# Kernel tuning notes

Hardware: AMD Instinct MI355X
Metric: run time of the kernel (lower is better)

The kernel has to match this reference:

```python
import jax, jax.numpy as jnp
import numpy as np
import math

EMB = 2048
HEADS = 16
HEAD_DIM = EMB // HEADS  # 128
SCALE = math.sqrt(HEAD_DIM)


def srms_norm(x, eps_min=1e-12):
    # Scaled RMS norm over last dim, computed in float32.
    d = x.shape[-1]
    xf = x.astype(jnp.float32)
    norm = jnp.linalg.norm(xf * (1.0 / math.sqrt(d)), axis=-1, keepdims=True)
    norm = jnp.maximum(norm, eps_min)
    return (xf / norm).astype(x.dtype)


def setup_inputs() -> dict:
    key = jax.random.key(0)
    ks = jax.random.split(key, 6)
    x = jax.random.normal(ks[0], (4, 4096, EMB), dtype=jnp.float32)
    # xavier-normal std for square D x D: sqrt(2/(D+D)) = 1/sqrt(D); gain=1 (lth=None)
    std = 1.0 / math.sqrt(EMB)
    Wq = jax.random.normal(ks[1], (EMB, EMB), dtype=jnp.float32) * std
    Wk = jax.random.normal(ks[2], (EMB, EMB), dtype=jnp.float32) * std
    Wv = jax.random.normal(ks[3], (EMB, EMB), dtype=jnp.float32) * std
    Wu = jax.random.normal(ks[4], (EMB, EMB), dtype=jnp.float32) * std
    Wo = jax.random.normal(ks[5], (EMB, EMB), dtype=jnp.float32) * std
    return {"x": x, "Wq": Wq, "Wk": Wk, "Wv": Wv, "Wu": Wu, "Wo": Wo}


def reference(x, Wq, Wk, Wv, Wu, Wo):
    B, L, D = x.shape
    H, dh = HEADS, HEAD_DIM
    # projections (weights stored as [in, out])
    q = (x @ Wq).reshape(B, L, H, dh).transpose(0, 2, 1, 3)  # [B,H,L,dh]
    k = (x @ Wk).reshape(B, L, H, dh).transpose(0, 2, 1, 3)
    v = (x @ Wv).reshape(B, L, H, dh).transpose(0, 2, 1, 3)
    u = (x @ Wu).reshape(B, L, H, dh).transpose(0, 2, 1, 3)
    q = jax.nn.relu(q) / SCALE
    k = jax.nn.relu(k) / SCALE
    u = jax.nn.silu(u)
    # linear retention: kv state [B,H,dh,dh], then q @ kv
    kv = jnp.einsum('bhlk,bhlv->bhkv', k, v)
    out = jnp.einsum('bhlk,bhkv->bhlv', q, kv)
    out = srms_norm(out) * u
    out = out.transpose(0, 2, 1, 3).reshape(B, L, D)
    return out @ Wo
```

## Files before the change

kernel.cpp:

```cpp
#include <hip/hip_runtime.h>
#include <hip/hip_bf16.h>
#include <cstdint>


typedef __attribute__((ext_vector_type(8))) short short8;
typedef __attribute__((ext_vector_type(4))) float f32x4;

#define DEVI static __device__ __forceinline__

DEVI float bf2f(unsigned short u) {
    union { unsigned int i; float f; } w; w.i = ((unsigned int)u) << 16; return w.f;
}
DEVI unsigned short f2bf(float f) {
    union { float f; unsigned int i; } w; w.f = f;
    return (unsigned short)((w.i + 0x7fffu + ((w.i >> 16) & 1u)) >> 16);
}

#define GLDS16(gp, lp) __builtin_amdgcn_global_load_lds( \
    (const __attribute__((address_space(1))) void*)(gp), \
    (__attribute__((address_space(3))) void*)(lp), 16, 0, 0)

__global__ void probe_dtype(const unsigned short* __restrict__ x, int* flag) {
    __shared__ int cnt;
    if (threadIdx.x == 0) cnt = 0;
    __syncthreads();
    int c = 0;
    for (int i = threadIdx.x; i < 4096; i += 256) {
        float a = fabsf(bf2f(x[i]));
        if (!(a <= 1e4f) || (a != 0.0f && a < 1e-4f)) ++c;
    }
    atomicAdd(&cnt, c);
    __syncthreads();
    if (threadIdx.x == 0) *flag = (cnt < 512) ? 1 : 0;
}

__global__ void wconvert(const void* __restrict__ Wq, const void* __restrict__ Wk,
                         const void* __restrict__ Wv, const void* __restrict__ Wu,
                         const void* __restrict__ Wo,
                         unsigned short* __restrict__ wt4,
                         unsigned short* __restrict__ wot,
                         const int* __restrict__ flag) {
    const int z = blockIdx.z;
    const void* W = (z == 0) ? Wq : (z == 1) ? Wk : (z == 2) ? Wv : (z == 3) ? Wu : Wo;
    const bool isbf = (*flag != 0);
    __shared__ float tile[32][33];
    const int j0 = blockIdx.x * 32, i0 = blockIdx.y * 32;
    const int tx = threadIdx.x, ty = threadIdx.y;
#pragma unroll
    for (int r = 0; r < 4; ++r) {
        const int i = i0 + ty * 4 + r;
        float v;
        if (isbf) v = bf2f(((const unsigned short*)W)[i * 2048 + j0 + tx]);
        else      v = ((const float*)W)[i * 2048 + j0 + tx];
        tile[ty * 4 + r][tx] = v;
    }
    __syncthreads();
#pragma unroll
    for (int r = 0; r < 4; ++r) {
        const int j = j0 + ty * 4 + r;
        const unsigned short bv = f2bf(tile[tx][ty * 4 + r]);
        if (z < 4) wt4[(long)(z * 2048 + j) * 2048 + i0 + tx] = bv;
        else       wot[(long)j * 2048 + i0 + tx] = bv;
    }
}

__global__ void xconvert(const void* __restrict__ X, unsigned short* __restrict__ xb,
                         const int* __restrict__ flag) {
    const bool isbf = (*flag != 0);
    const long i = (long)blockIdx.x * 256 + threadIdx.x;
    if (isbf) {
        ((uint4*)xb)[i] = ((const uint4*)X)[i];
    } else {
        const float4 f0 = ((const float4*)X)[2 * i];
        const float4 f1 = ((const float4*)X)[2 * i + 1];
        union { unsigned short us[8]; uint4 v; } o;
        o.us[0] = f2bf(f0.x); o.us[1] = f2bf(f0.y); o.us[2] = f2bf(f0.z); o.us[3] = f2bf(f0.w);
        o.us[4] = f2bf(f1.x); o.us[5] = f2bf(f1.y); o.us[6] = f2bf(f1.z); o.us[7] = f2bf(f1.w);
        ((uint4*)xb)[i] = o.v;
    }
}

DEVI void gemm_core(const unsigned short* __restrict__ Ag,
                    const unsigned short* __restrict__ Bg,
                    unsigned short* As, unsigned short* Bs,
                    f32x4 acc[8][4], const int tid) {
    const int wave = tid >> 6, lane = tid & 63;
    const int wr = wave >> 2, wc = wave & 3;
    const int srow = tid >> 2;
    const int lsl = (tid & 3) ^ ((srow >> 1) & 3);
    const unsigned short* ga0 = Ag + (long)srow * 2048 + lsl * 8;
    const unsigned short* ga1 = ga0 + 128 * 2048;
    const unsigned short* gb0 = Bg + (long)srow * 2048 + lsl * 8;
    const unsigned short* gb1 = gb0 + 128 * 2048;
    const int ldsb = wave * 512;

    const int psl = ((lane >> 4) ^ (((lane & 15) >> 1) & 3)) * 8;
    const int abase = (wr * 128 + (lane & 15)) * 32 + psl;
    const int bbase = (wc * 64 + (lane & 15)) * 32 + psl;

#define ISSUE(tt) do { const int _b = (tt) & 3; const int _ko = (tt) * 32; \
    GLDS16(ga0 + _ko, As + _b * 8192 + ldsb); \
    GLDS16(ga1 + _ko, As + _b * 8192 + 4096 + ldsb); \
    GLDS16(gb0 + _ko, Bs + _b * 8192 + ldsb); \
    GLDS16(gb1 + _ko, Bs + _b * 8192 + 4096 + ldsb); } while (0)
#define RDFRAG(aX, bX, buf) do { \
    const unsigned short* _a = As + (buf) * 8192; \
    const unsigned short* _b = Bs + (buf) * 8192; \
    _Pragma("unroll") for (int fm = 0; fm < 8; ++fm) aX[fm] = *(const short8*)(_a + abase + fm * 512); \
    _Pragma("unroll") for (int fn = 0; fn < 4; ++fn) bX[fn] = *(const short8*)(_b + bbase + fn * 512); } while (0)
#define MFMACL(aX, bX) do { \
    __builtin_amdgcn_s_setprio(1); \
    _Pragma("unroll") for (int fm = 0; fm < 8; ++fm) \
    _Pragma("unroll") for (int fn = 0; fn < 4; ++fn) \
        acc[fm][fn] = __builtin_amdgcn_mfma_f32_16x16x32_bf16(aX[fm], bX[fn], acc[fm][fn], 0, 0, 0); \
    __builtin_amdgcn_s_setprio(0); } while (0)

    ISSUE(0); ISSUE(1); ISSUE(2); ISSUE(3);
    asm volatile("s_waitcnt vmcnt(12)" ::: "memory");
    asm volatile("s_barrier" ::: "memory");
    short8 aE[8], bE[4], aO[8], bO[4];
    RDFRAG(aE, bE, 0);

    for (int tp = 0; tp < 32; ++tp) {
        const int t = 2 * tp;
        asm volatile("s_waitcnt vmcnt(8)" ::: "memory");
        asm volatile("s_barrier" ::: "memory");
        RDFRAG(aO, bO, (t + 1) & 3);
        asm volatile("s_waitcnt lgkmcnt(12)" ::: "memory");
        { int ti = t + 4; if (ti >= 64) ti -= 64; ISSUE(ti); }
        MFMACL(aE, bE);
        asm volatile("s_waitcnt vmcnt(8)" ::: "memory");
        asm volatile("s_barrier" ::: "memory");
        { int tr = t + 2; if (tr > 63) tr = 63; RDFRAG(aE, bE, tr & 3); }
        asm volatile("s_waitcnt lgkmcnt(12)" ::: "memory");
        { int ti = t + 5; if (ti >= 64) ti -= 64; ISSUE(ti); }
        MFMACL(aO, bO);
    }
    asm volatile("s_waitcnt vmcnt(0) lgkmcnt(0)" ::: "memory");
#undef ISSUE
#undef RDFRAG
#undef MFMACL
}

__global__ __launch_bounds__(512, 2)
void gemm_qkvu(const unsigned short* __restrict__ Xb,
               const unsigned short* __restrict__ Wt4,
               unsigned short* __restrict__ Qb, unsigned short* __restrict__ Kb,
               unsigned short* __restrict__ Vb, unsigned short* __restrict__ Ub) {
    __shared__ unsigned short As[4 * 8192];
    __shared__ unsigned short Bs[4 * 8192];
    const int orig = blockIdx.x;
    const int flat = (orig & 7) * 256 + (orig >> 3);
    const int mt = flat & 63, nt = flat >> 6;
    const long m0 = (long)mt * 256;
    const int tid = threadIdx.x;
    f32x4 acc[8][4] = {};

    gemm_core(Xb + m0 * 2048, Wt4 + (long)nt * 256 * 2048, As, Bs, acc, tid);

    const int wave = tid >> 6, lane = tid & 63;
    const int wr = wave >> 2, wc = wave & 3;
    const int seg = nt >> 3;
    unsigned short* outp = (seg == 0) ? Qb : (seg == 1) ? Kb : (seg == 2) ? Vb : Ub;
    const int cl0 = (nt & 7) * 256 + wc * 64;
#pragma unroll
    for (int fm = 0; fm < 8; ++fm) {
#pragma unroll
        for (int fn = 0; fn < 4; ++fn) {
            const int col = cl0 + fn * 16 + (lane & 15);
#pragma unroll
            for (int r = 0; r < 4; ++r) {
                const long row = m0 + wr * 128 + fm * 16 + ((lane >> 4) << 2) + r;
                float v = acc[fm][fn][r];
                if (seg <= 1)      v = fmaxf(v, 0.0f) * 0.08838834764831845f;
                else if (seg == 3) v = v / (1.0f + __expf(-v));
                outp[row * 2048 + col] = f2bf(v);
            }
        }
    }
}

__global__ __launch_bounds__(512, 2)
void gemm_out(const unsigned short* __restrict__ Obuf,
              const unsigned short* __restrict__ Wot,
              void* __restrict__ out, const int* __restrict__ flag) {
    __shared__ unsigned short As[4 * 8192];
    __shared__ unsigned short Bs[4 * 8192];
    const int orig = blockIdx.x;
    const int flat = (orig & 7) * 64 + (orig >> 3);
    const int mt = flat & 63, nt = flat >> 6;
    const long m0 = (long)mt * 256;
    const int j0 = nt * 256;
    const int tid = threadIdx.x;
    f32x4 acc[8][4] = {};

    gemm_core(Obuf + m0 * 2048, Wot + (long)j0 * 2048, As, Bs, acc, tid);

    const int wave = tid >> 6, lane = tid & 63;
    const int wr = wave >> 2, wc = wave & 3;
    const bool isbf = (*flag != 0);
#pragma unroll
    for (int fm = 0; fm < 8; ++fm) {
#pragma unroll
        for (int fn = 0; fn < 4; ++fn) {
            const int col = j0 + wc * 64 + fn * 16 + (lane & 15);
#pragma unroll
            for (int r = 0; r < 4; ++r) {
                const long row = m0 + wr * 128 + fm * 16 + ((lane >> 4) << 2) + r;
                const float v = acc[fm][fn][r];
                if (isbf) ((unsigned short*)out)[row * 2048 + col] = f2bf(v);
                else      ((float*)out)[row * 2048 + col] = v;
            }
        }
    }
}

__global__ void kv_accum(const unsigned short* __restrict__ Kb,
                         const unsigned short* __restrict__ Vb,
                         float* __restrict__ KVpart) {
    __shared__ unsigned short Kt[128 * 64];
    __shared__ unsigned short Vt[128 * 64];
    const int bh = blockIdx.x;
    const int chunk = blockIdx.y;
    const int b = bh >> 4, h = bh & 15;
    const int t = threadIdx.x, wave = t >> 6, lane = t & 63;
    const int wr = wave >> 1, wc = wave & 1;
    const int l0 = (t & 15) * 4;
    const int dkg = t >> 4;
    const long gbase = ((long)b * 4096 + chunk * 1024) * 2048 + h * 128;
    f32x4 acc[4][4] = {};

    for (int tile = 0; tile < 16; ++tile) {
        __syncthreads();
        short8 kr[4], vr[4];
#pragma unroll
        for (int li = 0; li < 4; ++li) {
            const long go = gbase + (long)(tile * 64 + l0 + li) * 2048 + dkg * 8;
            kr[li] = *(const short8*)(Kb + go);
            vr[li] = *(const short8*)(Vb + go);
        }
#pragma unroll
        for (int i = 0; i < 8; ++i) {
            const int row = dkg * 8 + i;
            const int lin = row * 128 + l0 * 2;
            const int off = (lin ^ ((row & 7) << 4)) >> 1;
            union { unsigned short us[4]; unsigned long long u; } pk, pv;
#pragma unroll
            for (int li = 0; li < 4; ++li) { pk.us[li] = (unsigned short)kr[li][i]; pv.us[li] = (unsigned short)vr[li][i]; }
            *(unsigned long long*)(Kt + off) = pk.u;
            *(unsigned long long*)(Vt + off) = pv.u;
        }
        __syncthreads();
#pragma unroll
        for (int ks = 0; ks < 2; ++ks) {
            const int kof = ks * 64 + (lane >> 4) * 16;
            short8 a[4], bfr[4];
#pragma unroll
            for (int f = 0; f < 4; ++f) {
                const int ra = wr * 64 + f * 16 + (lane & 15);
                const int rb = wc * 64 + f * 16 + (lane & 15);
                a[f]   = *(const short8*)(Vt + (((ra * 128 + kof) ^ ((ra & 7) << 4)) >> 1));
                bfr[f] = *(const short8*)(Kt + (((rb * 128 + kof) ^ ((rb & 7) << 4)) >> 1));
            }
#pragma unroll
            for (int fm = 0; fm < 4; ++fm)
#pragma unroll
                for (int fn = 0; fn < 4; ++fn)
                    acc[fm][fn] = __builtin_amdgcn_mfma_f32_16x16x32_bf16(a[fm], bfr[fn], acc[fm][fn], 0, 0, 0);
        }
    }
    float* dst = KVpart + ((long)chunk * 64 + bh) * 16384;
#pragma unroll
    for (int fm = 0; fm < 4; ++fm)
#pragma unroll
        for (int fn = 0; fn < 4; ++fn)
#pragma unroll
            for (int r = 0; r < 4; ++r) {
                const int dv = wr * 64 + fm * 16 + ((lane >> 4) << 2) + r;
                const int dk = wc * 64 + fn * 16 + (lane & 15);
                dst[dv * 128 + dk] = acc[fm][fn][r];
            }
}

__global__ void kv_finalize(const float* __restrict__ KVpart,
                            unsigned short* __restrict__ KVhi) {
    const long base = ((long)blockIdx.x * 256 + threadIdx.x) * 4;
    float4 s0 = *(const float4*)(KVpart + base);
    const float4 s1 = *(const float4*)(KVpart + 1048576 + base);
    const float4 s2 = *(const float4*)(KVpart + 2097152 + base);
    const float4 s3 = *(const float4*)(KVpart + 3145728 + base);
    float s[4] = { s0.x + s1.x + s2.x + s3.x, s0.y + s1.y + s2.y + s3.y,
                   s0.z + s1.z + s2.z + s3.z, s0.w + s1.w + s2.w + s3.w };
    union { unsigned short us[4]; unsigned long long u; } hi;
#pragma unroll
    for (int j = 0; j < 4; ++j) hi.us[j] = f2bf(s[j]);
    *(unsigned long long*)(KVhi + base) = hi.u;
}

__global__ void o_norm(const unsigned short* __restrict__ Qb,
                       const unsigned short* __restrict__ Ub,
                       const unsigned short* __restrict__ KVhi,
                       unsigned short* __restrict__ Ob) {
    __shared__ unsigned short Qs[128 * 128];
    const int tid = threadIdx.x, wave = tid >> 6, lane = tid & 63;
    const int tile = blockIdx.x;
    const int bh = blockIdx.y;
    const int b = bh >> 4, h = bh & 15;
    const long n0 = (long)b * 4096 + tile * 128;

    const int qrow = tid >> 4;
    const int qcol = (tid & 15) * 8;
#pragma unroll
    for (int i = 0; i < 8; ++i)
        GLDS16(Qb + (n0 + i * 16 + qrow) * 2048 + h * 128 + qcol, Qs + i * 2048 + wave * 512);
    __syncthreads();

    const unsigned short* KH = KVhi + (long)bh * 16384;
    f32x4 acc[2][8] = {};
#pragma unroll
    for (int kk = 0; kk < 4; ++kk) {
        const short8 a0 = *(const short8*)(Qs + (wave * 32 + (lane & 15)) * 128 + kk * 32 + (lane >> 4) * 8);
        const short8 a1 = *(const short8*)(Qs + (wave * 32 + 16 + (lane & 15)) * 128 + kk * 32 + (lane >> 4) * 8);
#pragma unroll
        for (int fn = 0; fn < 8; ++fn) {
            const int bo = (fn * 16 + (lane & 15)) * 128 + kk * 32 + (lane >> 4) * 8;
            const short8 bhi = *(const short8*)(KH + bo);
            acc[0][fn] = __builtin_amdgcn_mfma_f32_16x16x32_bf16(a0, bhi, acc[0][fn], 0, 0, 0);
            acc[1][fn] = __builtin_amdgcn_mfma_f32_16x16x32_bf16(a1, bhi, acc[1][fn], 0, 0, 0);
        }
    }

#pragma unroll
    for (int fm = 0; fm < 2; ++fm) {
#pragma unroll
        for (int r = 0; r < 4; ++r) {
            float ssq = 0.0f;
#pragma unroll
            for (int fn = 0; fn < 8; ++fn) { const float v = acc[fm][fn][r]; ssq += v * v; }
            ssq += __shfl_xor(ssq, 1);
            ssq += __shfl_xor(ssq, 2);
            ssq += __shfl_xor(ssq, 4);
            ssq += __shfl_xor(ssq, 8);
            const float nrm = fmaxf(sqrtf(ssq) * 0.08838834764831845f, 1e-12f);
            const float scl = 1.0f / nrm;
            const long row = n0 + wave * 32 + fm * 16 + ((lane >> 4) << 2) + r;
#pragma unroll
            for (int fn = 0; fn < 8; ++fn) {
                const int col = fn * 16 + (lane & 15);
                const float uv = bf2f(Ub[row * 2048 + h * 128 + col]);
                Ob[row * 2048 + h * 128 + col] = f2bf(acc[fm][fn][r] * scl * uv);
            }
        }
    }
}

extern "C" void kernel_launch(void* const* d_in, const int* in_sizes, int n_in,
                              void* d_out, int out_size, void* d_ws, size_t ws_size,
                              hipStream_t stream) {
    (void)in_sizes; (void)n_in; (void)out_size; (void)ws_size;
    char* ws = (char*)d_ws;
    unsigned short* Xb  = (unsigned short*)(ws + 0);
    unsigned short* Wt4 = (unsigned short*)(ws + 67108864);
    unsigned short* Wot = (unsigned short*)(ws + 100663296);
    unsigned short* Qb  = (unsigned short*)(ws + 109051904);
    unsigned short* Kb  = (unsigned short*)(ws + 176160768);
    unsigned short* Vb  = (unsigned short*)(ws + 243269632);
    unsigned short* Ub  = (unsigned short*)(ws + 310378496);
    int*            flag= (int*)(ws + 381681664);
    float*          KVpart = (float*)Wt4;
    unsigned short* KVhi   = (unsigned short*)(ws + 67108864 + 16777216);
    unsigned short* Ob     = Xb;

    probe_dtype<<<1, 256, 0, stream>>>((const unsigned short*)d_in[0], flag);
    wconvert<<<dim3(64, 64, 5), dim3(32, 8), 0, stream>>>(d_in[1], d_in[2], d_in[3],
                                                          d_in[4], d_in[5], Wt4, Wot, flag);
    xconvert<<<16384, 256, 0, stream>>>(d_in[0], Xb, flag);
    gemm_qkvu<<<2048, 512, 0, stream>>>(Xb, Wt4, Qb, Kb, Vb, Ub);
    kv_accum<<<dim3(64, 4), 256, 0, stream>>>(Kb, Vb, KVpart);
    kv_finalize<<<1024, 256, 0, stream>>>(KVpart, KVhi);
    o_norm<<<dim3(32, 64), 256, 0, stream>>>(Qb, Ub, KVhi, Ob);
    gemm_out<<<512, 512, 0, stream>>>(Ob, Wot, d_out, flag);
}
```

Before: 979.4 us.

## Stage GEMM and norm epilogues through swizzled LDS for vectorized stores

The QKVU and output GEMM epilogues now write accumulator fragments into XOR-swizzled shared memory (reusing the A/B tiles) and then emit 16-byte coalesced global stores instead of scattered 2- or 4-byte stores. The o_norm kernel loads U into LDS with global_load_lds, swizzles the Q/U tiles, and writes its output through LDS with vector stores. kv_accum changes its thread mapping and swizzle to cut LDS bank conflicts. This adds barriers and extra LDS traffic in exchange for far fewer, wider global memory transactions.

```diff
diff --git a/kernel.cpp b/kernel.cpp
--- a/kernel.cpp
+++ b/kernel.cpp
@@ -163,20 +163,33 @@
     const int seg = nt >> 3;
     unsigned short* outp = (seg == 0) ? Qb : (seg == 1) ? Kb : (seg == 2) ? Vb : Ub;
     const int cl0 = (nt & 7) * 256 + wc * 64;
+
+    __syncthreads();
+    unsigned short* reg = (wave < 4 ? As : Bs) + (wave & 3) * 8192;
 #pragma unroll
     for (int fm = 0; fm < 8; ++fm) {
 #pragma unroll
         for (int fn = 0; fn < 4; ++fn) {
-            const int col = cl0 + fn * 16 + (lane & 15);
 #pragma unroll
             for (int r = 0; r < 4; ++r) {
-                const long row = m0 + wr * 128 + fm * 16 + ((lane >> 4) << 2) + r;
+                const int lrow = fm * 16 + ((lane >> 4) << 2) + r;
+                const int lcol = fn * 16 + (lane & 15);
                 float v = acc[fm][fn][r];
                 if (seg <= 1)      v = fmaxf(v, 0.0f) * 0.08838834764831845f;
                 else if (seg == 3) v = v / (1.0f + __expf(-v));
-                outp[row * 2048 + col] = f2bf(v);
+                const int ofs = lrow * 64 + ((((lcol >> 3) ^ ((lrow >> 2) & 7)) << 3) | (lcol & 7));
+                reg[ofs] = f2bf(v);
             }
         }
+    }
+#pragma unroll
+    for (int p = 0; p < 16; ++p) {
+        const int row = p * 8 + (lane >> 3);
+        const int slotL = lane & 7;
+        const uint4 val = *(const uint4*)(reg + row * 64 + slotL * 8);
+        const long grow = m0 + wr * 128 + row;
+        const int gcol = cl0 + ((slotL ^ ((row >> 2) & 7)) << 3);
+        *(uint4*)(outp + grow * 2048 + gcol) = val;
     }
 }
 
@@ -199,17 +212,57 @@
     const int wave = tid >> 6, lane = tid & 63;
     const int wr = wave >> 2, wc = wave & 3;
     const bool isbf = (*flag != 0);
-#pragma unroll
-    for (int fm = 0; fm < 8; ++fm) {
-#pragma unroll
-        for (int fn = 0; fn < 4; ++fn) {
-            const int col = j0 + wc * 64 + fn * 16 + (lane & 15);
-#pragma unroll
-            for (int r = 0; r < 4; ++r) {
-                const long row = m0 + wr * 128 + fm * 16 + ((lane >> 4) << 2) + r;
-                const float v = acc[fm][fn][r];
-                if (isbf) ((unsigned short*)out)[row * 2048 + col] = f2bf(v);
-                else      ((float*)out)[row * 2048 + col] = v;
+    __syncthreads();
+    unsigned short* reg = (wave < 4 ? As : Bs) + (wave & 3) * 8192;
+
+    if (isbf) {
+        unsigned short* outp = (unsigned short*)out;
+        const int cl0 = j0 + wc * 64;
+#pragma unroll
+        for (int fm = 0; fm < 8; ++fm)
+#pragma unroll
+            for (int fn = 0; fn < 4; ++fn)
+#pragma unroll
+                for (int r = 0; r < 4; ++r) {
+                    const int lrow = fm * 16 + ((lane >> 4) << 2) + r;
+                    const int lcol = fn * 16 + (lane & 15);
+                    const int ofs = lrow * 64 + ((((lcol >> 3) ^ ((lrow >> 2) & 7)) << 3) | (lcol & 7));
+                    reg[ofs] = f2bf(acc[fm][fn][r]);
+                }
+#pragma unroll
+        for (int p = 0; p < 16; ++p) {
+            const int row = p * 8 + (lane >> 3);
+            const int slotL = lane & 7;
+            const uint4 val = *(const uint4*)(reg + row * 64 + slotL * 8);
+            const long grow = m0 + wr * 128 + row;
+            const int gcol = cl0 + ((slotL ^ ((row >> 2) & 7)) << 3);
+            *(uint4*)(outp + grow * 2048 + gcol) = val;
+        }
+    } else {
+        float* outf = (float*)out;
+        float* regf = (float*)reg;
+#pragma unroll
+        for (int h = 0; h < 2; ++h) {
+#pragma unroll
+            for (int fm = 0; fm < 8; ++fm)
+#pragma unroll
+                for (int fnh = 0; fnh < 2; ++fnh)
+#pragma unroll
+                    for (int r = 0; r < 4; ++r) {
+                        const int fn = h * 2 + fnh;
+                        const int lrow = fm * 16 + ((lane >> 4) << 2) + r;
+                        const int lcolf = fnh * 16 + (lane & 15);
+                        const int ofs = lrow * 32 + ((((lcolf >> 2) ^ ((lrow >> 2) & 7)) << 2) | (lcolf & 3));
+                        regf[ofs] = acc[fm][fn][r];
+                    }
+#pragma unroll
+            for (int p = 0; p < 16; ++p) {
+                const int row = p * 8 + (lane >> 3);
+                const int slotL = lane & 7;
+                const float4 val = *(const float4*)(regf + row * 32 + slotL * 4);
+                const long grow = m0 + wr * 128 + row;
+                const int gcol = j0 + wc * 64 + h * 32 + ((slotL ^ ((row >> 2) & 7)) << 2);
+                *(float4*)(outf + grow * 2048 + gcol) = val;
             }
         }
     }
@@ -225,8 +278,8 @@
     const int b = bh >> 4, h = bh & 15;
     const int t = threadIdx.x, wave = t >> 6, lane = t & 63;
     const int wr = wave >> 1, wc = wave & 1;
-    const int l0 = (t & 15) * 4;
-    const int dkg = t >> 4;
+    const int dkg = t & 15;
+    const int l0 = (t >> 4) * 4;
     const long gbase = ((long)b * 4096 + chunk * 1024) * 2048 + h * 128;
     f32x4 acc[4][4] = {};
 
@@ -243,7 +296,7 @@
         for (int i = 0; i < 8; ++i) {
             const int row = dkg * 8 + i;
             const int lin = row * 128 + l0 * 2;
-            const int off = (lin ^ ((row & 7) << 4)) >> 1;
+            const int off = (lin ^ ((((row) ^ (row >> 3)) & 7) << 4)) >> 1;
             union { unsigned short us[4]; unsigned long long u; } pk, pv;
 #pragma unroll
             for (int li = 0; li < 4; ++li) { pk.us[li] = (unsigned short)kr[li][i]; pv.us[li] = (unsigned short)vr[li][i]; }
@@ -259,8 +312,8 @@
             for (int f = 0; f < 4; ++f) {
                 const int ra = wr * 64 + f * 16 + (lane & 15);
                 const int rb = wc * 64 + f * 16 + (lane & 15);
-                a[f]   = *(const short8*)(Vt + (((ra * 128 + kof) ^ ((ra & 7) << 4)) >> 1));
-                bfr[f] = *(const short8*)(Kt + (((rb * 128 + kof) ^ ((rb & 7) << 4)) >> 1));
+                a[f]   = *(const short8*)(Vt + (((ra * 128 + kof) ^ ((((ra) ^ (ra >> 3)) & 7) << 4)) >> 1));
+                bfr[f] = *(const short8*)(Kt + (((rb * 128 + kof) ^ ((((rb) ^ (rb >> 3)) & 7) << 4)) >> 1));
             }
 #pragma unroll
             for (int fm = 0; fm < 4; ++fm)
@@ -302,6 +355,7 @@
                        const unsigned short* __restrict__ KVhi,
                        unsigned short* __restrict__ Ob) {
     __shared__ unsigned short Qs[128 * 128];
+    __shared__ unsigned short Us[128 * 128];
     const int tid = threadIdx.x, wave = tid >> 6, lane = tid & 63;
     const int tile = blockIdx.x;
     const int bh = blockIdx.y;
@@ -309,18 +363,25 @@
     const long n0 = (long)b * 4096 + tile * 128;
 
     const int qrow = tid >> 4;
-    const int qcol = (tid & 15) * 8;
-#pragma unroll
-    for (int i = 0; i < 8; ++i)
-        GLDS16(Qb + (n0 + i * 16 + qrow) * 2048 + h * 128 + qcol, Qs + i * 2048 + wave * 512);
+#pragma unroll
+    for (int i = 0; i < 8; ++i) {
+        const int row = i * 16 + qrow;
+        const int scol = ((tid & 15) ^ ((row >> 2) & 7)) * 8;
+        GLDS16(Qb + (n0 + row) * 2048 + h * 128 + scol, Qs + i * 2048 + wave * 512);
+        GLDS16(Ub + (n0 + row) * 2048 + h * 128 + scol, Us + i * 2048 + wave * 512);
+    }
     __syncthreads();
 
     const unsigned short* KH = KVhi + (long)bh * 16384;
     f32x4 acc[2][8] = {};
+    const int arow0 = wave * 32 + (lane & 15);
+    const int arow1 = arow0 + 16;
+    const int fq0 = (arow0 >> 2) & 7;
+    const int fq1 = (arow1 >> 2) & 7;
 #pragma unroll
     for (int kk = 0; kk < 4; ++kk) {
-        const short8 a0 = *(const short8*)(Qs + (wave * 32 + (lane & 15)) * 128 + kk * 32 + (lane >> 4) * 8);
-        const short8 a1 = *(const short8*)(Qs + (wave * 32 + 16 + (lane & 15)) * 128 + kk * 32 + (lane >> 4) * 8);
+        const short8 a0 = *(const short8*)(Qs + arow0 * 128 + (((kk * 4 + (lane >> 4)) ^ fq0) << 3));
+        const short8 a1 = *(const short8*)(Qs + arow1 * 128 + (((kk * 4 + (lane >> 4)) ^ fq1) << 3));
 #pragma unroll
         for (int fn = 0; fn < 8; ++fn) {
             const int bo = (fn * 16 + (lane & 15)) * 128 + kk * 32 + (lane >> 4) * 8;
@@ -343,14 +404,25 @@
             ssq += __shfl_xor(ssq, 8);
             const float nrm = fmaxf(sqrtf(ssq) * 0.08838834764831845f, 1e-12f);
             const float scl = 1.0f / nrm;
-            const long row = n0 + wave * 32 + fm * 16 + ((lane >> 4) << 2) + r;
+            const int lrow = wave * 32 + fm * 16 + ((lane >> 4) << 2) + r;
+            const int fr = (lrow >> 2) & 7;
 #pragma unroll
             for (int fn = 0; fn < 8; ++fn) {
                 const int col = fn * 16 + (lane & 15);
-                const float uv = bf2f(Ub[row * 2048 + h * 128 + col]);
-                Ob[row * 2048 + h * 128 + col] = f2bf(acc[fm][fn][r] * scl * uv);
+                const int sofs = lrow * 128 + ((((col >> 3) ^ fr) << 3) | (col & 7));
+                const float uv = bf2f(Us[sofs]);
+                Qs[sofs] = f2bf(acc[fm][fn][r] * scl * uv);
             }
         }
+    }
+    __syncthreads();
+#pragma unroll
+    for (int p = 0; p < 8; ++p) {
+        const int row = p * 16 + (tid >> 4);
+        const int slotL = tid & 15;
+        const uint4 val = *(const uint4*)(Qs + row * 128 + slotL * 8);
+        const int gcol = ((slotL ^ ((row >> 2) & 7)) & 15) * 8;
+        *(uint4*)(Ob + (n0 + row) * 2048 + h * 128 + gcol) = val;
     }
 }
 
```

After: 1.004 ms. 1.03x slower.
